# Performance work log

Measured on AMD Instinct MI355X. Metric: run time of the kernel, lower is better.

Reference implementation:

```python
import jax, jax.numpy as jnp
import numpy as np

# J2 (von Mises) plane-strain elastoplasticity with linear isotropic hardening
# (faithful stand-in for pyprnn's J2Material: elastic predictor + radial return,
#  committed history = plastic strain tensor + accumulated plastic strain).
E_MOD = 3130.0   # Young's modulus (epoxy, MPa)
NU = 0.37        # Poisson ratio
SIG_Y = 64.8     # initial yield stress
H_ISO = 300.0    # linear isotropic hardening modulus
MU = E_MOD / (2.0 * (1.0 + NU))
LAM = E_MOD * NU / ((1.0 + NU) * (1.0 - 2.0 * NU))


def j2_update(eps, eps_p, alpha):
    """eps: [P,3] (exx, eyy, gamma_xy engineering); eps_p: [P,4] (xx,yy,zz,xy tensorial);
    alpha: [P] accumulated plastic strain. Returns (stress [P,3], eps_p_new, alpha_new)."""
    ee_xx = eps[:, 0] - eps_p[:, 0]
    ee_yy = eps[:, 1] - eps_p[:, 1]
    ee_zz = -eps_p[:, 2]                      # plane strain: total ezz = 0
    ee_xy = 0.5 * eps[:, 2] - eps_p[:, 3]     # tensorial shear
    tr = ee_xx + ee_yy + ee_zz
    # trial (elastic predictor) stress
    sxx = LAM * tr + 2.0 * MU * ee_xx
    syy = LAM * tr + 2.0 * MU * ee_yy
    szz = LAM * tr + 2.0 * MU * ee_zz
    sxy = 2.0 * MU * ee_xy
    p = (sxx + syy + szz) / 3.0
    dxx, dyy, dzz = sxx - p, syy - p, szz - p
    q = jnp.sqrt(1.5 * (dxx * dxx + dyy * dyy + dzz * dzz + 2.0 * sxy * sxy))
    f = q - (SIG_Y + H_ISO * alpha)
    dgam = jnp.maximum(f, 0.0) / (3.0 * MU + H_ISO)   # radial return, closed form
    qs = jnp.maximum(q, 1e-12)
    nxx, nyy, nzz, nxy = 1.5 * dxx / qs, 1.5 * dyy / qs, 1.5 * dzz / qs, 1.5 * sxy / qs
    two_mu_dg = 2.0 * MU * dgam
    sig = jnp.stack([sxx - two_mu_dg * nxx, syy - two_mu_dg * nyy, sxy - two_mu_dg * nxy], axis=-1)
    eps_p_new = eps_p + dgam[:, None] * jnp.stack([nxx, nyy, nzz, nxy], axis=-1)
    alpha_new = alpha + dgam
    return sig, eps_p_new, alpha_new


def setup_inputs() -> dict:
    key = jax.random.key(0)
    k1, k2, k3 = jax.random.split(key, 3)
    B, T, F = 16384, 128, 3
    MATPTS = 16
    L, O = MATPTS * F, 3
    x = jax.random.normal(k1, (B, T, F), dtype=jnp.float32) * 0.02  # strain paths
    W1 = jax.random.normal(k2, (L, F), dtype=jnp.float32) * (1.0 / np.sqrt(F))
    W2 = jax.random.normal(k3, (O, L), dtype=jnp.float32) * (1.0 / np.sqrt(L))
    return {"x": x, "W1": W1, "W2": W2}


def reference(x, W1, W2):
    B, T, F = x.shape
    L = W1.shape[0]
    P = B * (L // F)                 # total material points = batch * mat_pts
    W2s = jax.nn.softplus(W2)        # SoftLayer: positive weights, no bias
    xt = jnp.swapaxes(x, 0, 1)       # [T, B, F]

    def step(carry, xi):
        eps_p, alpha = carry
        lat = xi @ W1.T                       # fc1 (no bias): [B, L]
        eps = lat.reshape(P, F)               # per-material-point strain
        sig, eps_p, alpha = j2_update(eps, eps_p, alpha)   # update + commit
        out = sig.reshape(B, L) @ W2s.T       # fc2 softplus-weighted linear
        return (eps_p, alpha), out

    carry0 = (jnp.zeros((P, 4), jnp.float32), jnp.zeros((P,), jnp.float32))
    _, ys = jax.lax.scan(step, carry0, xt)    # ys: [T, B, O]
    return jnp.swapaxes(ys, 0, 1)             # [B, T, O]
```

## Files before the change

kernel.cpp:

```cpp
#include <hip/hip_runtime.h>
#include <math.h>


#define BLOCK 256
#define BPB 32
#define TSTEPS 128
#define ROWF (TSTEPS * 3)

typedef float v2 __attribute__((ext_vector_type(2)));

static __device__ __forceinline__ v2 vfma(v2 a, v2 b, v2 c) {
    return __builtin_elementwise_fma(a, b, c);
}
static __device__ __forceinline__ v2 vmax(v2 a, v2 b) {
    return __builtin_elementwise_max(a, b);
}

#define DPP_ADDST(v, ctrl)                                                   \
    v += __int_as_float(__builtin_amdgcn_update_dpp(                         \
        0, __float_as_int(v), (ctrl), 0xf, 0xf, true))
#define RED8(v)                                                              \
    do { DPP_ADDST(v, 0xB1); DPP_ADDST(v, 0x4E); DPP_ADDST(v, 0x141); } while (0)

#define DPP_ST(r, ctrl) "v_add_f32_dpp %" #r ", %" #r ", %" #r " " ctrl \
                        " row_mask:0xf bank_mask:0xf\n\t"
#define DPP_STAGE(ctrl) \
    DPP_ST(0, ctrl) DPP_ST(1, ctrl) DPP_ST(2, ctrl)  DPP_ST(3, ctrl) \
    DPP_ST(4, ctrl) DPP_ST(5, ctrl) DPP_ST(6, ctrl)  DPP_ST(7, ctrl) \
    DPP_ST(8, ctrl) DPP_ST(9, ctrl) DPP_ST(10, ctrl) DPP_ST(11, ctrl)
#define DPP_BFLY12(a0,a1,a2,a3,a4,a5,a6,a7,a8,a9,a10,a11)                    \
  asm volatile(                                                              \
    "s_nop 1\n\t"                                                            \
    DPP_STAGE("quad_perm:[1,0,3,2]")                                         \
    DPP_STAGE("quad_perm:[2,3,0,1]")                                         \
    DPP_STAGE("row_half_mirror")                                             \
    : "+v"(a0), "+v"(a1), "+v"(a2), "+v"(a3), "+v"(a4), "+v"(a5),            \
      "+v"(a6), "+v"(a7), "+v"(a8), "+v"(a9), "+v"(a10), "+v"(a11))

__global__ __launch_bounds__(BLOCK, 2)
void prnn_j2_kernel(const float* __restrict__ x,
                    const float* __restrict__ W1,
                    const float* __restrict__ W2,
                    float* __restrict__ out)
{
    constexpr float MU    = (float)(3130.0 / (2.0 * (1.0 + 0.37)));
    constexpr float LAM   = (float)(3130.0 * 0.37 / ((1.0 + 0.37) * (1.0 - 2.0 * 0.37)));
    constexpr float SIG_Y = 64.8f;
    constexpr float H_ISO = 300.0f;
    const float TWO_MU  = 2.0f * MU;
    const float INV_DEN = 1.0f / (3.0f * MU + H_ISO);
    const float K3P     = (3.0f * MU) * INV_DEN;
    const float HP      = H_ISO * INV_DEN;
    const float CSC     = 1.0f / (MU * 2.4494897427831781f);
    const float Y0      = SIG_Y * CSC;

    const int tid = threadIdx.x;
    const int g   = tid >> 3;
    const int l   = tid & 7;
    const int gb  = blockIdx.x * BPB + g;

    const float* xb = x + gb * ROWF;
    float* ob = out + gb * ROWF;

    const int pa = l, pb = l + 8;
    v2 w1p[3][3], w2p[3][3];
    #pragma unroll
    for (int c = 0; c < 3; ++c)
        #pragma unroll
        for (int f = 0; f < 3; ++f) {
            float s = (c == 2) ? 0.5f : 1.0f;
            w1p[c][f].x = s * W1[(3 * pa + c) * 3 + f];
            w1p[c][f].y = s * W1[(3 * pb + c) * 3 + f];
        }
    #pragma unroll
    for (int o = 0; o < 3; ++o)
        #pragma unroll
        for (int c = 0; c < 3; ++c) {
            float wa = W2[o * 48 + 3 * pa + c];
            float wb = W2[o * 48 + 3 * pb + c];
            w2p[o][c].x = fmaxf(wa, 0.0f) + log1pf(expf(-fabsf(wa)));
            w2p[o][c].y = fmaxf(wb, 0.0f) + log1pf(expf(-fabsf(wb)));
        }

    float Mrow[3];
    {
        float Ms[3][3];
        #pragma unroll
        for (int f = 0; f < 3; ++f) {
            v2 ax = (LAM + TWO_MU) * w1p[0][f] + LAM * w1p[1][f];
            v2 ay = LAM * w1p[0][f] + (LAM + TWO_MU) * w1p[1][f];
            v2 as = TWO_MU * w1p[2][f];
            #pragma unroll
            for (int o = 0; o < 3; ++o) {
                v2 mp = vfma(w2p[o][0], ax, vfma(w2p[o][1], ay, w2p[o][2] * as));
                float ms = mp.x + mp.y;
                RED8(ms);
                Ms[o][f] = ms;
            }
        }
        #pragma unroll
        for (int f = 0; f < 3; ++f) {
            float v = (l == 0) ? Ms[0][f] : ((l == 1) ? Ms[1][f] : Ms[2][f]);
            Mrow[f] = v;
        }
    }

    v2 p0 = {0.f,0.f}, p1 = {0.f,0.f}, p2 = {0.f,0.f}, p3 = {0.f,0.f};
    v2 Y  = {Y0, Y0};
    v2 z0 = {0.f,0.f}, z1 = {0.f,0.f}, z2 = {0.f,0.f};

    const float4* xv = (const float4*)xb;
    const bool wact = (l < 3);
    float* obl = ob + l;

#define J2_PHYS(x0_, x1_, x2_, rr, mxv)                                      \
  {                                                                          \
    const float x0s = (x0_), x1s = (x1_), x2s = (x2_);                       \
    const v2 x0 = {x0s, x0s}, x1 = {x1s, x1s}, x2 = {x2s, x2s};              \
    const v2 ee_xx = vfma(w1p[0][0], x0, vfma(w1p[0][1], x1,                 \
                          vfma(w1p[0][2], x2, -p0)));                        \
    const v2 ee_yy = vfma(w1p[1][0], x0, vfma(w1p[1][1], x1,                 \
                          vfma(w1p[1][2], x2, -p1)));                        \
    const v2 ee_xy = vfma(w1p[2][0], x0, vfma(w1p[2][1], x1,                 \
                          vfma(w1p[2][2], x2, -p3)));                        \
    const v2 tr = (ee_xx + ee_yy) - p2;                                      \
    const v2 c3 = tr * (1.0f / 3.0f);                                        \
    const v2 exd = ee_xx - c3;                                               \
    const v2 eyd = ee_yy - c3;                                               \
    const v2 szd = exd + eyd;                                    \
    const v2 t2 = ee_xy * ee_xy;                                             \
    v2 u = exd * exd;                                                        \
    u = vfma(eyd, eyd, u);                                                   \
    u = vfma(szd, szd, u);                                                   \
    u = vfma(t2, (v2){2.0f, 2.0f}, u);                                       \
    u = vmax(u, (v2){1e-30f, 1e-30f});                                       \
    v2 rq;                                                                   \
    rq.x = __builtin_amdgcn_rsqf(u.x);                                       \
    rq.y = __builtin_amdgcn_rsqf(u.y);                                       \
    const v2 su = u * rq;                                       \
    const v2 fY = vmax(su - Y, (v2){0.0f, 0.0f});                            \
    Y = vfma((v2){HP, HP}, fY, Y);                                           \
    const v2 k = (K3P * fY) * rq;                                            \
    const v2 kdx = k * exd;                                                  \
    const v2 kdy = k * eyd;                                                  \
    const v2 kdxy = k * ee_xy;                                               \
    p0 += kdx;                                                               \
    p1 += kdy;                                                               \
    p3 += kdxy;                                                              \
    p2 = p2 - k * szd;                                                       \
    z0 = vfma(w2p[0][0], kdx, vfma(w2p[0][1], kdy, vfma(w2p[0][2], kdxy, z0)));\
    z1 = vfma(w2p[1][0], kdx, vfma(w2p[1][1], kdy, vfma(w2p[1][2], kdxy, z1)));\
    z2 = vfma(w2p[2][0], kdx, vfma(w2p[2][1], kdy, vfma(w2p[2][2], kdxy, z2)));\
    (rr)[0] = z0.x + z0.y;                                                   \
    (rr)[1] = z1.x + z1.y;                                                   \
    (rr)[2] = z2.x + z2.y;                                                   \
    (mxv) = fmaf(Mrow[0], x0s, fmaf(Mrow[1], x1s, Mrow[2] * x2s));           \
  }

    float4 A0 = xv[0], A1 = xv[1], A2 = xv[2];

    for (int tb = 0; tb < TSTEPS / 4; ++tb) {
        const int nb = (tb < TSTEPS / 4 - 1) ? (3 * tb + 3) : (3 * tb);
        float4 An0 = xv[nb + 0];
        float4 An1 = xv[nb + 1];
        float4 An2 = xv[nb + 2];

        float r[12], mx[4];
        J2_PHYS(A0.x,  A0.y,  A0.z,  r + 0, mx[0]);
        J2_PHYS(A0.w,  A1.x,  A1.y,  r + 3, mx[1]);
        J2_PHYS(A1.z,  A1.w,  A2.x,  r + 6, mx[2]);
        J2_PHYS(A2.y,  A2.z,  A2.w,  r + 9, mx[3]);

        DPP_BFLY12(r[0], r[1], r[2], r[3], r[4], r[5],
                   r[6], r[7], r[8], r[9], r[10], r[11]);

        if (wact) {
            float zz0 = (l == 0) ? r[0] : ((l == 1) ? r[1]  : r[2]);
            float zz1 = (l == 0) ? r[3] : ((l == 1) ? r[4]  : r[5]);
            float zz2 = (l == 0) ? r[6] : ((l == 1) ? r[7]  : r[8]);
            float zz3 = (l == 0) ? r[9] : ((l == 1) ? r[10] : r[11]);
            obl[12 * tb + 0] = fmaf(-TWO_MU, zz0, mx[0]);
            obl[12 * tb + 3] = fmaf(-TWO_MU, zz1, mx[1]);
            obl[12 * tb + 6] = fmaf(-TWO_MU, zz2, mx[2]);
            obl[12 * tb + 9] = fmaf(-TWO_MU, zz3, mx[3]);
        }

        A0 = An0; A1 = An1; A2 = An2;
    }
#undef J2_PHYS
}

extern "C" void kernel_launch(void* const* d_in, const int* in_sizes, int n_in,
                              void* d_out, int out_size, void* d_ws, size_t ws_size,
                              hipStream_t stream) {
    const float* x  = (const float*)d_in[0];
    const float* W1 = (const float*)d_in[1];
    const float* W2 = (const float*)d_in[2];
    float* out = (float*)d_out;

    const int B = 16384;
    dim3 grid(B / BPB);
    dim3 block(BLOCK);
    prnn_j2_kernel<<<grid, block, 0, stream>>>(x, W1, W2, out);
}
```

Baseline: 117.0 us.

## Map one material point per lane with 16-lane groups instead of packed pairs

Each batch row now uses 16 lanes, one material point per lane, where it previously used 8 lanes each handling two points with packed v2 math. The output reduction gains a fourth DPP stage (row_mirror) to cover all 16 lanes, and launch bounds rise to 4 blocks per SM with half as many batch rows per block. The deviatoric algebra is also regrouped so the W1·x terms and c3 are formed before subtracting the plastic state. The aim is more parallelism and lower per-thread register pressure. The cost is twice as many threads, each loading x redundantly, plus an extra reduction stage per step.

After: 138.5 us. 18.4% more time.

```diff
diff --git a/kernel.cpp b/kernel.cpp
--- a/kernel.cpp
+++ b/kernel.cpp
@@ -3,24 +3,16 @@
 
 
 #define BLOCK 256
-#define BPB 32
+#define BPB 16
 #define TSTEPS 128
 #define ROWF (TSTEPS * 3)
-
-typedef float v2 __attribute__((ext_vector_type(2)));
-
-static __device__ __forceinline__ v2 vfma(v2 a, v2 b, v2 c) {
-    return __builtin_elementwise_fma(a, b, c);
-}
-static __device__ __forceinline__ v2 vmax(v2 a, v2 b) {
-    return __builtin_elementwise_max(a, b);
-}
 
 #define DPP_ADDST(v, ctrl)                                                   \
     v += __int_as_float(__builtin_amdgcn_update_dpp(                         \
         0, __float_as_int(v), (ctrl), 0xf, 0xf, true))
-#define RED8(v)                                                              \
-    do { DPP_ADDST(v, 0xB1); DPP_ADDST(v, 0x4E); DPP_ADDST(v, 0x141); } while (0)
+#define RED16(v)                                                             \
+    do { DPP_ADDST(v, 0xB1); DPP_ADDST(v, 0x4E);                             \
+         DPP_ADDST(v, 0x141); DPP_ADDST(v, 0x140); } while (0)
 
 #define DPP_ST(r, ctrl) "v_add_f32_dpp %" #r ", %" #r ", %" #r " " ctrl \
                         " row_mask:0xf bank_mask:0xf\n\t"
@@ -34,10 +26,11 @@
     DPP_STAGE("quad_perm:[1,0,3,2]")                                         \
     DPP_STAGE("quad_perm:[2,3,0,1]")                                         \
     DPP_STAGE("row_half_mirror")                                             \
+    DPP_STAGE("row_mirror")                                                  \
     : "+v"(a0), "+v"(a1), "+v"(a2), "+v"(a3), "+v"(a4), "+v"(a5),            \
       "+v"(a6), "+v"(a7), "+v"(a8), "+v"(a9), "+v"(a10), "+v"(a11))
 
-__global__ __launch_bounds__(BLOCK, 2)
+__global__ __launch_bounds__(BLOCK, 4)
 void prnn_j2_kernel(const float* __restrict__ x,
                     const float* __restrict__ W1,
                     const float* __restrict__ W2,
@@ -55,31 +48,27 @@
     const float Y0      = SIG_Y * CSC;
 
     const int tid = threadIdx.x;
-    const int g   = tid >> 3;
-    const int l   = tid & 7;
+    const int g   = tid >> 4;
+    const int l   = tid & 15;
     const int gb  = blockIdx.x * BPB + g;
 
     const float* xb = x + gb * ROWF;
     float* ob = out + gb * ROWF;
 
-    const int pa = l, pb = l + 8;
-    v2 w1p[3][3], w2p[3][3];
+    float w1p[3][3], w2p[3][3];
     #pragma unroll
     for (int c = 0; c < 3; ++c)
         #pragma unroll
         for (int f = 0; f < 3; ++f) {
             float s = (c == 2) ? 0.5f : 1.0f;
-            w1p[c][f].x = s * W1[(3 * pa + c) * 3 + f];
-            w1p[c][f].y = s * W1[(3 * pb + c) * 3 + f];
+            w1p[c][f] = s * W1[(3 * l + c) * 3 + f];
         }
     #pragma unroll
     for (int o = 0; o < 3; ++o)
         #pragma unroll
         for (int c = 0; c < 3; ++c) {
-            float wa = W2[o * 48 + 3 * pa + c];
-            float wb = W2[o * 48 + 3 * pb + c];
-            w2p[o][c].x = fmaxf(wa, 0.0f) + log1pf(expf(-fabsf(wa)));
-            w2p[o][c].y = fmaxf(wb, 0.0f) + log1pf(expf(-fabsf(wb)));
+            float w = W2[o * 48 + 3 * l + c];
+            w2p[o][c] = fmaxf(w, 0.0f) + log1pf(expf(-fabsf(w)));
         }
 
     float Mrow[3];
@@ -87,14 +76,14 @@
         float Ms[3][3];
         #pragma unroll
         for (int f = 0; f < 3; ++f) {
-            v2 ax = (LAM + TWO_MU) * w1p[0][f] + LAM * w1p[1][f];
-            v2 ay = LAM * w1p[0][f] + (LAM + TWO_MU) * w1p[1][f];
-            v2 as = TWO_MU * w1p[2][f];
+            float ax = (LAM + TWO_MU) * w1p[0][f] + LAM * w1p[1][f];
+            float ay = LAM * w1p[0][f] + (LAM + TWO_MU) * w1p[1][f];
+            float as = TWO_MU * w1p[2][f];
             #pragma unroll
             for (int o = 0; o < 3; ++o) {
-                v2 mp = vfma(w2p[o][0], ax, vfma(w2p[o][1], ay, w2p[o][2] * as));
-                float ms = mp.x + mp.y;
-                RED8(ms);
+                float ms = fmaf(w2p[o][0], ax,
+                           fmaf(w2p[o][1], ay, w2p[o][2] * as));
+                RED16(ms);
                 Ms[o][f] = ms;
             }
         }
@@ -105,9 +94,9 @@
         }
     }
 
-    v2 p0 = {0.f,0.f}, p1 = {0.f,0.f}, p2 = {0.f,0.f}, p3 = {0.f,0.f};
-    v2 Y  = {Y0, Y0};
-    v2 z0 = {0.f,0.f}, z1 = {0.f,0.f}, z2 = {0.f,0.f};
+    float p0 = 0.f, p1 = 0.f, p2 = 0.f, p3 = 0.f;
+    float Y  = Y0;
+    float z0 = 0.f, z1 = 0.f, z2 = 0.f;
 
     const float4* xv = (const float4*)xb;
     const bool wact = (l < 3);
@@ -115,46 +104,41 @@
 
 #define J2_PHYS(x0_, x1_, x2_, rr, mxv)                                      \
   {                                                                          \
-    const float x0s = (x0_), x1s = (x1_), x2s = (x2_);                       \
-    const v2 x0 = {x0s, x0s}, x1 = {x1s, x1s}, x2 = {x2s, x2s};              \
-    const v2 ee_xx = vfma(w1p[0][0], x0, vfma(w1p[0][1], x1,                 \
-                          vfma(w1p[0][2], x2, -p0)));                        \
-    const v2 ee_yy = vfma(w1p[1][0], x0, vfma(w1p[1][1], x1,                 \
-                          vfma(w1p[1][2], x2, -p1)));                        \
-    const v2 ee_xy = vfma(w1p[2][0], x0, vfma(w1p[2][1], x1,                 \
-                          vfma(w1p[2][2], x2, -p3)));                        \
-    const v2 tr = (ee_xx + ee_yy) - p2;                                      \
-    const v2 c3 = tr * (1.0f / 3.0f);                                        \
-    const v2 exd = ee_xx - c3;                                               \
-    const v2 eyd = ee_yy - c3;                                               \
-    const v2 szd = exd + eyd;                                    \
-    const v2 t2 = ee_xy * ee_xy;                                             \
-    v2 u = exd * exd;                                                        \
-    u = vfma(eyd, eyd, u);                                                   \
-    u = vfma(szd, szd, u);                                                   \
-    u = vfma(t2, (v2){2.0f, 2.0f}, u);                                       \
-    u = vmax(u, (v2){1e-30f, 1e-30f});                                       \
-    v2 rq;                                                                   \
-    rq.x = __builtin_amdgcn_rsqf(u.x);                                       \
-    rq.y = __builtin_amdgcn_rsqf(u.y);                                       \
-    const v2 su = u * rq;                                       \
-    const v2 fY = vmax(su - Y, (v2){0.0f, 0.0f});                            \
-    Y = vfma((v2){HP, HP}, fY, Y);                                           \
-    const v2 k = (K3P * fY) * rq;                                            \
-    const v2 kdx = k * exd;                                                  \
-    const v2 kdy = k * eyd;                                                  \
-    const v2 kdxy = k * ee_xy;                                               \
+    const float x0 = (x0_), x1 = (x1_), x2 = (x2_);                          \
+    const float wx0 = fmaf(w1p[0][0], x0, fmaf(w1p[0][1], x1, w1p[0][2]*x2));\
+    const float wx1 = fmaf(w1p[1][0], x0, fmaf(w1p[1][1], x1, w1p[1][2]*x2));\
+    const float wxy = fmaf(w1p[2][0], x0, fmaf(w1p[2][1], x1, w1p[2][2]*x2));\
+    const float c3  = (wx0 + wx1) * (1.0f / 3.0f);                           \
+    const float ex0 = wx0 - c3;                                              \
+    const float ey0 = wx1 - c3;                                              \
+    const float exd = ex0 - p0;                                              \
+    const float eyd = ey0 - p1;                                              \
+    const float exy = wxy - p3;                                              \
+    const float szd = p2 + c3;                                   \
+    const float t2  = exy * exy;                                             \
+    const float ua  = fmaf(eyd, eyd, exd * exd);                             \
+    const float ub  = fmaf(t2, 2.0f, szd * szd);                             \
+    float u = ua + ub;                                                       \
+    u = fmaxf(u, 1e-30f);                                                    \
+    const float rq = __builtin_amdgcn_rsqf(u);                               \
+    const float su = u * rq;                                    \
+    const float fY = fmaxf(su - Y, 0.0f);                                    \
+    Y = fmaf(HP, fY, Y);                                                     \
+    const float k = (K3P * fY) * rq;                                         \
+    const float kdx  = k * exd;                                              \
+    const float kdy  = k * eyd;                                              \
+    const float kdxy = k * exy;                                              \
     p0 += kdx;                                                               \
     p1 += kdy;                                                               \
     p3 += kdxy;                                                              \
-    p2 = p2 - k * szd;                                                       \
-    z0 = vfma(w2p[0][0], kdx, vfma(w2p[0][1], kdy, vfma(w2p[0][2], kdxy, z0)));\
-    z1 = vfma(w2p[1][0], kdx, vfma(w2p[1][1], kdy, vfma(w2p[1][2], kdxy, z1)));\
-    z2 = vfma(w2p[2][0], kdx, vfma(w2p[2][1], kdy, vfma(w2p[2][2], kdxy, z2)));\
-    (rr)[0] = z0.x + z0.y;                                                   \
-    (rr)[1] = z1.x + z1.y;                                                   \
-    (rr)[2] = z2.x + z2.y;                                                   \
-    (mxv) = fmaf(Mrow[0], x0s, fmaf(Mrow[1], x1s, Mrow[2] * x2s));           \
+    p2 = fmaf(-k, szd, p2);                                                  \
+    z0 = fmaf(w2p[0][0], kdx, fmaf(w2p[0][1], kdy, fmaf(w2p[0][2], kdxy, z0)));\
+    z1 = fmaf(w2p[1][0], kdx, fmaf(w2p[1][1], kdy, fmaf(w2p[1][2], kdxy, z1)));\
+    z2 = fmaf(w2p[2][0], kdx, fmaf(w2p[2][1], kdy, fmaf(w2p[2][2], kdxy, z2)));\
+    (rr)[0] = z0;                                                            \
+    (rr)[1] = z1;                                                            \
+    (rr)[2] = z2;                                                            \
+    (mxv) = fmaf(Mrow[0], x0, fmaf(Mrow[1], x1, Mrow[2] * x2));              \
   }
 
     float4 A0 = xv[0], A1 = xv[1], A2 = xv[2];
```
